# Optimization experiments

Hardware: AMD Instinct MI355X
Metric: run time of the kernel (lower is better)

The kernel has to match this reference:

```python
import jax, jax.numpy as jnp
import numpy as np

THRE = 4.0  # ReLUX threshold / multispike lens
EPS = 1e-5  # BatchNorm eps (torch default)

@jax.custom_vjp
def spike(x):
    # multispike forward: floor(clamp(x,0,4)+0.5)
    return jnp.floor(jnp.clip(x, 0.0, THRE) + 0.5)

def _spike_fwd(x):
    return spike(x), x

def _spike_bwd(x, g):
    # surrogate gradient: pass-through on 0 < x < lens
    return (g * ((x > 0) & (x < THRE)).astype(g.dtype),)

spike.defvjp(_spike_fwd, _spike_bwd)


def setup_inputs() -> dict:
    key = jax.random.key(0)
    k0, k1, k2 = jax.random.split(key, 3)
    B, N, C = 4, 1024, 512
    x = jax.random.normal(k0, (B, N, C), jnp.float32)
    Wqkv = jax.random.normal(k1, (3 * C, C), jnp.float32) * (C ** -0.5)  # Linear weight [out,in], no bias
    gamma = jnp.ones((3 * C,), jnp.float32)   # BN weight
    beta = jnp.zeros((3 * C,), jnp.float32)   # BN bias
    Wproj = jax.random.normal(k2, (C, C), jnp.float32) * (C ** -0.5)
    bproj = jnp.zeros((C,), jnp.float32)
    return {"x": x, "Wqkv": Wqkv, "gamma": gamma, "beta": beta, "Wproj": Wproj, "bproj": bproj}


def reference(x, Wqkv, gamma, beta, Wproj, bproj):
    B, N, C = x.shape
    H = 8
    hd = C // H
    scale = hd ** -0.5

    xs = spike(x)                                    # head_spike
    qkv = jnp.einsum('bnc,dc->bnd', xs, Wqkv)        # [B,N,3C]
    # BatchNorm1d over channel dim with batch stats across (B, N)
    mu = qkv.mean(axis=(0, 1))
    var = qkv.var(axis=(0, 1))
    qkv = (qkv - mu) * jax.lax.rsqrt(var + EPS) * gamma + beta

    qkv = qkv.reshape(B, N, 3, H, hd).transpose(2, 0, 3, 1, 4)  # [3,B,H,N,hd]
    q = spike(qkv[0])
    k = spike(qkv[1])
    v = spike(qkv[2])

    attn = jnp.einsum('bhnd,bhmd->bhnm', q, k)       # no softmax
    attn = spike(attn)
    out = jnp.einsum('bhnm,bhmd->bhnd', attn, v) * scale
    out = out.transpose(0, 2, 1, 3).reshape(B, N, C)
    out = spike(out)                                 # project_spike
    return jnp.einsum('bnc,dc->bnd', out, Wproj) + bproj
```

## Files before the change

### kernel.cpp

```cpp
#include <hip/hip_runtime.h>

typedef __attribute__((ext_vector_type(8))) short short8;
typedef __attribute__((ext_vector_type(4))) short short4v;
typedef __attribute__((ext_vector_type(8))) signed char s8x8;
typedef __attribute__((ext_vector_type(4))) unsigned char u8x4;
typedef __attribute__((ext_vector_type(4))) float f32x4;
typedef __attribute__((ext_vector_type(4))) int int4v;
typedef __attribute__((ext_vector_type(4))) unsigned int u32x4;

#define THRE 4.0f

#define GLOAD_LDS16(g, l) \
    __builtin_amdgcn_global_load_lds((const __attribute__((address_space(1))) void*)(g), \
                                     (__attribute__((address_space(3))) void*)(l), 16, 0, 0)

__device__ __forceinline__ float spikef(float x) {
    return floorf(fminf(fmaxf(x, 0.0f), THRE) + 0.5f);
}
__device__ __forceinline__ unsigned short f2bf(float f) {
    return (unsigned short)(__builtin_bit_cast(unsigned int, f) >> 16);
}
__device__ __forceinline__ unsigned short f2bf_rn(float f) {
    unsigned u = __builtin_bit_cast(unsigned int, f);
    unsigned r = ((u >> 16) & 1u) + 0x7FFFu;
    return (unsigned short)((u + r) >> 16);
}
__device__ __forceinline__ float bf2f(unsigned short s) {
    return __builtin_bit_cast(float, (unsigned int)s << 16);
}
__device__ __forceinline__ int4v mfma_i8(u32x4 a, u32x4 b, int4v c) {
    return __builtin_amdgcn_mfma_i32_16x16x64_i8(__builtin_bit_cast(int4v, a),
                                                 __builtin_bit_cast(int4v, b), c, 0, 0, 0);
}

__global__ void k_prep(const float* __restrict__ x,
                       const float* __restrict__ Wq, const float* __restrict__ Wp,
                       unsigned char* __restrict__ xs8, signed char* __restrict__ Wq8,
                       float* __restrict__ wscale, short* __restrict__ Wpd) {
    const int blk = blockIdx.x, tid = threadIdx.x;
    if (blk < 2048) {
        const int i = blk * 256 + tid;
        const float4 v = *(const float4*)&x[(size_t)i * 4];
        u8x4 o;
        o.x = (unsigned char)spikef(v.x);
        o.y = (unsigned char)spikef(v.y);
        o.z = (unsigned char)spikef(v.z);
        o.w = (unsigned char)spikef(v.w);
        *(u8x4*)&xs8[(size_t)i * 4] = o;
    } else if (blk < 2432) {
        const int row = (blk - 2048) * 4 + (tid >> 6);
        const int lane = tid & 63;
        const float* wr = Wq + (size_t)row * 512 + lane * 8;
        float w[8];
        float mx = 0.f;
        #pragma unroll
        for (int i = 0; i < 8; ++i) { w[i] = wr[i]; mx = fmaxf(mx, fabsf(w[i])); }
        #pragma unroll
        for (int o = 32; o > 0; o >>= 1) mx = fmaxf(mx, __shfl_xor(mx, o, 64));
        const float inv = mx > 0.f ? 127.0f / mx : 0.f;
        s8x8 q;
        #pragma unroll
        for (int i = 0; i < 8; ++i) q[i] = (signed char)rintf(w[i] * inv);
        *(s8x8*)&Wq8[(size_t)row * 512 + lane * 8] = q;
        if (lane == 0) wscale[row] = mx > 0.f ? mx / 127.0f : 0.f;
    } else {
        const int i = (blk - 2432) * 256 + tid;
        const float4 v = *(const float4*)&Wp[(size_t)i * 4];
        short4v o;
        o.x = (short)(__builtin_bit_cast(unsigned int, v.x) >> 16);
        o.y = (short)(__builtin_bit_cast(unsigned int, v.y) >> 16);
        o.z = (short)(__builtin_bit_cast(unsigned int, v.z) >> 16);
        o.w = (short)(__builtin_bit_cast(unsigned int, v.w) >> 16);
        *(short4v*)&Wpd[(size_t)i * 4] = o;
    }
}

__global__ __launch_bounds__(256) void k_gemm_qkv(const unsigned char* __restrict__ A,
                                                  const signed char* __restrict__ B,
                                                  const float* __restrict__ wscale,
                                                  short* __restrict__ C,
                                                  float* __restrict__ psum,
                                                  float* __restrict__ psq) {
    __shared__ __align__(16) unsigned char As[128 * 128];
    __shared__ __align__(16) unsigned char Bs[96 * 128];
    const int tid  = threadIdx.x;
    const int lane = tid & 63, wv = tid >> 6;
    const int wy = wv >> 1, wx = wv & 1;
    const int quad = lane >> 4, l16 = lane & 15;
    const int u = blockIdx.x;
    const int mtile = u & 31;
    const int m0 = mtile * 128, n0 = (u >> 5) * 96;
    const int N = 1536;

    int4v acc[4][3];
    #pragma unroll
    for (int i = 0; i < 4; ++i)
        #pragma unroll
        for (int j = 0; j < 3; ++j)
            #pragma unroll
            for (int r = 0; r < 4; ++r) acc[i][j][r] = 0;

    const unsigned char* gA[4]; unsigned char* lA[4];
    #pragma unroll
    for (int i = 0; i < 4; ++i) {
        int L = wv + 4 * i;
        int c = L * 64 + lane;
        int r = c >> 3, g = (c & 7) ^ (r & 7);
        gA[i] = A + (size_t)(m0 + r) * 512 + g * 16;
        lA[i] = &As[(size_t)c * 16];
    }
    const unsigned char* gB[3]; unsigned char* lB[3];
    #pragma unroll
    for (int i = 0; i < 3; ++i) {
        int L = wv + 4 * i;
        int c = L * 64 + lane;
        int r = c >> 3, g = (c & 7) ^ (r & 7);
        gB[i] = (const unsigned char*)B + (size_t)(n0 + r) * 512 + g * 16;
        lB[i] = &Bs[(size_t)c * 16];
    }

    for (int k0 = 0; k0 < 512; k0 += 128) {
        __syncthreads();
        #pragma unroll
        for (int i = 0; i < 4; ++i) GLOAD_LDS16(gA[i] + k0, lA[i]);
        #pragma unroll
        for (int i = 0; i < 3; ++i) GLOAD_LDS16(gB[i] + k0, lB[i]);
        __syncthreads();
        #pragma unroll
        for (int kk = 0; kk < 2; ++kk) {
            u32x4 aF[4], bF[3];
            #pragma unroll
            for (int mt = 0; mt < 4; ++mt) {
                const int r = wy * 64 + mt * 16 + l16;
                aF[mt] = *(const u32x4*)&As[(size_t)r * 128 + (((kk * 4 + quad) ^ (r & 7)) * 16)];
            }
            #pragma unroll
            for (int nt = 0; nt < 3; ++nt) {
                const int r = wx * 48 + nt * 16 + l16;
                bF[nt] = *(const u32x4*)&Bs[(size_t)r * 128 + (((kk * 4 + quad) ^ (r & 7)) * 16)];
            }
            #pragma unroll
            for (int mt = 0; mt < 4; ++mt)
                #pragma unroll
                for (int nt = 0; nt < 3; ++nt)
                    acc[mt][nt] = mfma_i8(aF[mt], bF[nt], acc[mt][nt]);
        }
    }

    float sc[3];
    #pragma unroll
    for (int nt = 0; nt < 3; ++nt) sc[nt] = wscale[n0 + wx * 48 + nt * 16 + l16];

    float vacc[4][3][4];
    #pragma unroll
    for (int mt = 0; mt < 4; ++mt)
        #pragma unroll
        for (int r = 0; r < 4; ++r) {
            int row = m0 + wy * 64 + mt * 16 + quad * 4 + r;
            short* Cr = C + (size_t)row * N + n0 + wx * 48 + l16;
            #pragma unroll
            for (int nt = 0; nt < 3; ++nt) {
                float v = (float)acc[mt][nt][r] * sc[nt];
                vacc[mt][nt][r] = v;
                Cr[nt * 16] = (short)f2bf_rn(v);
            }
        }

    __syncthreads();
    float* PS = (float*)As;
    float* PQ = (float*)Bs;
    #pragma unroll
    for (int nt = 0; nt < 3; ++nt) {
        float s = 0.f, q = 0.f;
        #pragma unroll
        for (int mt = 0; mt < 4; ++mt)
            #pragma unroll
            for (int r = 0; r < 4; ++r) {
                float v = vacc[mt][nt][r];
                s += v;
                q = fmaf(v, v, q);
            }
        PS[(wy * 4 + quad) * 96 + wx * 48 + nt * 16 + l16] = s;
        PQ[(wy * 4 + quad) * 96 + wx * 48 + nt * 16 + l16] = q;
    }
    __syncthreads();
    if (tid < 96) {
        float s = 0.f, q = 0.f;
        #pragma unroll
        for (int i = 0; i < 8; ++i) { s += PS[i * 96 + tid]; q += PQ[i * 96 + tid]; }
        psum[mtile * 1536 + n0 + tid] = s;
        psq [mtile * 1536 + n0 + tid] = q;
    }
}

__global__ __launch_bounds__(256) void k_gemm_proj(const short* __restrict__ A,
                                                   const short* __restrict__ B,
                                                   const float* __restrict__ bias,
                                                   float* __restrict__ C) {
    __shared__ __align__(16) short As[32 * 64];
    __shared__ __align__(16) short Bs[128 * 64];
    const int tid  = threadIdx.x;
    const int lane = tid & 63, wv = tid >> 6;
    const int wy = wv >> 1, wx = wv & 1;
    const int quad = lane >> 4, l16 = lane & 15;
    const int u = blockIdx.x;
    const int mtile = u & 127;
    const int m0 = mtile * 32, n0 = (u >> 7) * 128;
    const int K = 512, N = 512;

    f32x4 acc[4];
    #pragma unroll
    for (int j = 0; j < 4; ++j)
        #pragma unroll
        for (int r = 0; r < 4; ++r) acc[j][r] = 0.f;

    const short* gA0; short* lA0;
    {
        int c = tid;
        int r = c >> 3, g = (c & 7) ^ (r & 7);
        gA0 = A + (size_t)(m0 + r) * K + g * 8;
        lA0 = &As[(size_t)c * 8];
    }
    const short* gB[4]; short* lB[4];
    #pragma unroll
    for (int i = 0; i < 4; ++i) {
        int c = tid + 256 * i;
        int r = c >> 3, g = (c & 7) ^ (r & 7);
        gB[i] = B + (size_t)(n0 + r) * K + g * 8;
        lB[i] = &Bs[(size_t)c * 8];
    }

    for (int k0 = 0; k0 < K; k0 += 64) {
        __syncthreads();
        GLOAD_LDS16(gA0 + k0, lA0);
        #pragma unroll
        for (int i = 0; i < 4; ++i) GLOAD_LDS16(gB[i] + k0, lB[i]);
        __syncthreads();
        #pragma unroll
        for (int kk = 0; kk < 2; ++kk) {
            const int ra = wy * 16 + l16;
            short8 aF = *(const short8*)&As[(size_t)ra * 64 + (((kk * 4 + quad) ^ (ra & 7)) * 8)];
            #pragma unroll
            for (int nt = 0; nt < 4; ++nt) {
                const int rb = wx * 64 + nt * 16 + l16;
                short8 bF = *(const short8*)&Bs[(size_t)rb * 64 + (((kk * 4 + quad) ^ (rb & 7)) * 8)];
                acc[nt] = __builtin_amdgcn_mfma_f32_16x16x32_bf16(aF, bF, acc[nt], 0, 0, 0);
            }
        }
    }

    float bs[4];
    #pragma unroll
    for (int nt = 0; nt < 4; ++nt) bs[nt] = bias[n0 + wx * 64 + nt * 16 + l16];
    #pragma unroll
    for (int r = 0; r < 4; ++r) {
        int row = m0 + wy * 16 + quad * 4 + r;
        float* Cr = C + (size_t)row * N + n0 + wx * 64 + l16;
        #pragma unroll
        for (int nt = 0; nt < 4; ++nt) Cr[nt * 16] = acc[nt][r] + bs[nt];
    }
}

__global__ __launch_bounds__(256) void k_bn_spike(const short* __restrict__ qkvb,
                           const float* __restrict__ psum, const float* __restrict__ psq,
                           const float* __restrict__ gamma, const float* __restrict__ beta,
                           unsigned char* __restrict__ qp, unsigned char* __restrict__ kp,
                           unsigned char* __restrict__ vt) {
    __shared__ float sa[64], sb[64];
    __shared__ __align__(16) unsigned char tile[64 * 80];
    const int tid = threadIdx.x;
    const int slice = blockIdx.x;
    const int c0 = slice * 64;
    const int r0 = blockIdx.y * 256;
    const int b = r0 >> 10, nb = r0 & 1023;

    if (tid < 64) {
        const int c = c0 + tid;
        double s = 0.0, q = 0.0;
        for (int st = 0; st < 32; ++st) { s += (double)psum[st * 1536 + c]; q += (double)psq[st * 1536 + c]; }
        const double mu  = s / 4096.0;
        const double var = q / 4096.0 - mu * mu;
        const float a = (float)((double)gamma[c] / sqrt(var + 1e-5));
        sa[tid] = a;
        sb[tid] = fmaf(-(float)mu, a, beta[c]);
    }
    __syncthreads();

    if (slice < 16) {
        const int h = slice & 7;
        const int ch4 = (tid & 15) * 4, rr = tid >> 4;
        const float4 A4 = *(const float4*)&sa[ch4];
        const float4 B4 = *(const float4*)&sb[ch4];
        unsigned char* base = (slice < 8 ? qp : kp) + (((size_t)b * 8 + h) * 1024 + nb) * 64;
        for (int i = rr; i < 256; i += 16) {
            const short4v v4 = *(const short4v*)&qkvb[(size_t)(r0 + i) * 1536 + c0 + ch4];
            u8x4 o;
            o.x = (unsigned char)spikef(fmaf(bf2f((unsigned short)v4.x), A4.x, B4.x));
            o.y = (unsigned char)spikef(fmaf(bf2f((unsigned short)v4.y), A4.y, B4.y));
            o.z = (unsigned char)spikef(fmaf(bf2f((unsigned short)v4.z), A4.z, B4.z));
            o.w = (unsigned char)spikef(fmaf(bf2f((unsigned short)v4.w), A4.w, B4.w));
            *(u8x4*)&base[(size_t)i * 64 + ch4] = o;
        }
    } else {
        const int h = slice - 16;
        const int ch = tid & 63, rq = tid >> 6;
        const float A = sa[ch], Bsh = sb[ch];
        const int e = tid >> 2, j0 = (tid & 3) * 16;
        unsigned char* vbase = vt + (((size_t)b * 8 + h) * 64 + e) * 1024 + nb;
        for (int rb = 0; rb < 4; ++rb) {
            __syncthreads();
            for (int i = rq; i < 64; i += 4) {
                float v = bf2f((unsigned short)qkvb[(size_t)(r0 + rb * 64 + i) * 1536 + c0 + ch]);
                tile[ch * 80 + i] = (unsigned char)spikef(fmaf(v, A, Bsh));
            }
            __syncthreads();
            *(u32x4*)&vbase[rb * 64 + j0] = *(const u32x4*)&tile[e * 80 + j0];
        }
    }
}

__global__ __launch_bounds__(256) void k_attn(const unsigned char* __restrict__ qp,
                                              const unsigned char* __restrict__ kp,
                                              const unsigned char* __restrict__ vt,
                                              short* __restrict__ sout) {
    __shared__ __align__(16) unsigned char SM[54272];
    unsigned char* Qs = SM;
    unsigned char* Ks = SM + 4096;
    unsigned char* Vs = SM + 20480;
    unsigned int* Sb = (unsigned int*)(SM + 36864);
    const int tid  = threadIdx.x;
    const int lane = tid & 63, w = tid >> 6;
    const int quad = lane >> 4, l16 = lane & 15;
    const int u = blockIdx.x;
    const int bhid = u & 31;
    const int b = bhid >> 3, h = bhid & 7;
    const int n0 = (u >> 5) * 64;
    const size_t bh = (size_t)b * 8 + h;

    {
        const int r = tid >> 2, p = tid & 3;
        const int g = p ^ (r & 3) ^ ((r >> 2) & 3);
        GLOAD_LDS16(qp + (bh * 1024 + n0 + r) * 64 + g * 16, Qs + (size_t)tid * 16);
    }
    const unsigned char* gK[4]; unsigned char* lK[4];
    const unsigned char* gV[4]; unsigned char* lV[4];
    #pragma unroll
    for (int i = 0; i < 4; ++i) {
        int c = tid + 256 * i;
        int rk = c >> 2, pk2 = c & 3;
        int gk = pk2 ^ (rk & 3) ^ ((rk >> 2) & 3);
        gK[i] = kp + (bh * 1024 + rk) * 64 + gk * 16;
        lK[i] = Ks + (size_t)c * 16;
        int rv = c >> 4, pv = c & 15;
        int gv = pv ^ (rv & 15);
        gV[i] = vt + (bh * 64 + rv) * 1024 + gv * 16;
        lV[i] = Vs + (size_t)c * 16;
    }
    __syncthreads();
    u32x4 qf[4];
    {
        const int pq = quad ^ (l16 & 3) ^ ((l16 >> 2) & 3);
        #pragma unroll
        for (int mt = 0; mt < 4; ++mt)
            qf[mt] = *(const u32x4*)&Qs[(mt * 16 + l16) * 64 + pq * 16];
    }

    int4v of[4];
    #pragma unroll
    for (int mt = 0; mt < 4; ++mt)
        #pragma unroll
        for (int r = 0; r < 4; ++r) of[mt][r] = 0;

    const int pk = quad ^ (l16 & 3) ^ ((l16 >> 2) & 3);

    for (int j0 = 0; j0 < 1024; j0 += 256) {
        __syncthreads();
        #pragma unroll
        for (int i = 0; i < 4; ++i) {
            GLOAD_LDS16(gK[i] + (size_t)j0 * 64, lK[i]);
            GLOAD_LDS16(gV[i] + j0, lV[i]);
        }
        __syncthreads();

        #pragma unroll
        for (int jt = 0; jt < 4; ++jt) {
            u32x4 kf = *(const u32x4*)&Ks[(w * 64 + jt * 16 + l16) * 64 + pk * 16];
            #pragma unroll
            for (int mt = 0; mt < 4; ++mt) {
                int4v z;
                #pragma unroll
                for (int r = 0; r < 4; ++r) z[r] = 0;
                int4v s = mfma_i8(kf, qf[mt], z);
                unsigned int pkk = 0;
                #pragma unroll
                for (int r = 0; r < 4; ++r) {
                    int v = s[r]; v = v < 0 ? 0 : (v > 4 ? 4 : v);
                    pkk |= (unsigned int)v << (8 * r);
                }
                Sb[(mt * 16 + l16) * 68 + w * 16 + jt * 4 + quad] = pkk;
            }
        }
        __syncthreads();

        #pragma unroll
        for (int kk = 0; kk < 4; ++kk) {
            const int pv = (kk * 4 + quad) ^ l16;
            u32x4 bV = *(const u32x4*)&Vs[(w * 16 + l16) * 256 + pv * 16];
            #pragma unroll
            for (int mt = 0; mt < 4; ++mt) {
                u32x4 aS = *(const u32x4*)&Sb[(mt * 16 + l16) * 68 + kk * 16 + quad * 4];
                of[mt] = mfma_i8(aS, bV, of[mt]);
            }
        }
    }

    #pragma unroll
    for (int mt = 0; mt < 4; ++mt)
        #pragma unroll
        for (int r = 0; r < 4; ++r) {
            size_t orow = (size_t)b * 1024 + n0 + mt * 16 + quad * 4 + r;
            sout[orow * 512 + h * 64 + w * 16 + l16] =
                (short)f2bf(spikef((float)of[mt][r] * 0.125f));
        }
}

extern "C" void kernel_launch(void* const* d_in, const int* in_sizes, int n_in,
                              void* d_out, int out_size, void* d_ws, size_t ws_size,
                              hipStream_t stream) {
    const float* x     = (const float*)d_in[0];
    const float* Wqkv  = (const float*)d_in[1];
    const float* gamma = (const float*)d_in[2];
    const float* beta  = (const float*)d_in[3];
    const float* Wproj = (const float*)d_in[4];
    const float* bproj = (const float*)d_in[5];
    float* out = (float*)d_out;

    char* w = (char*)d_ws;
    unsigned char* xs8   = (unsigned char*)(w);
    signed char* Wq8     = (signed char*)(w + 8388608);
    float* wscale        = (float*)(w + 9437184);
    short* Wproj2        = (short*)(w + 11534336);
    short* qkvb          = (short*)(w + 12582912);
    unsigned char* qp    = (unsigned char*)(w + 37748736);
    unsigned char* kp    = (unsigned char*)(w + 41943040);
    unsigned char* vt    = (unsigned char*)(w + 46137344);
    float* psum          = (float*)(w + 50331648);
    float* psq           = psum + 32 * 1536;
    short* sout          = (short*)(w);

    k_prep<<<2688, 256, 0, stream>>>(x, Wqkv, Wproj, xs8, Wq8, wscale, Wproj2);
    k_gemm_qkv<<<512, 256, 0, stream>>>(xs8, Wq8, wscale, qkvb, psum, psq);
    k_bn_spike<<<dim3(24, 16), 256, 0, stream>>>(qkvb, psum, psq, gamma, beta, qp, kp, vt);
    k_attn<<<512, 256, 0, stream>>>(qp, kp, vt, sout);
    k_gemm_proj<<<512, 256, 0, stream>>>(sout, Wproj2, bproj, out);
}
```

Before: 110.3 us.

## Load K/V fragments directly from global into registers, double-buffer score tile

The attention kernel no longer stages Q, K and V through shared memory via global_load_lds. Each wave instead reads its MFMA fragments straight from global memory into registers, prefetching the next K chunk while the current one is processed. The V-transpose producer now writes V in a blocked layout that matches those register loads, and the score buffer is double-buffered with s_setprio hints around the MFMA sections. The Wproj bf16 conversion also switches from truncation to round-to-nearest. This removes LDS traffic and a pair of barriers per chunk, in exchange for more uncoalesced global loads and higher register pressure.

Result: no change. 108.9 us (-1.2%).

```diff
diff --git a/kernel.cpp b/kernel.cpp
--- a/kernel.cpp
+++ b/kernel.cpp
@@ -67,10 +67,10 @@
         const int i = (blk - 2432) * 256 + tid;
         const float4 v = *(const float4*)&Wp[(size_t)i * 4];
         short4v o;
-        o.x = (short)(__builtin_bit_cast(unsigned int, v.x) >> 16);
-        o.y = (short)(__builtin_bit_cast(unsigned int, v.y) >> 16);
-        o.z = (short)(__builtin_bit_cast(unsigned int, v.z) >> 16);
-        o.w = (short)(__builtin_bit_cast(unsigned int, v.w) >> 16);
+        o.x = (short)f2bf_rn(v.x);
+        o.y = (short)f2bf_rn(v.y);
+        o.z = (short)f2bf_rn(v.z);
+        o.w = (short)f2bf_rn(v.w);
         *(short4v*)&Wpd[(size_t)i * 4] = o;
     }
 }
@@ -306,7 +306,8 @@
         const int ch = tid & 63, rq = tid >> 6;
         const float A = sa[ch], Bsh = sb[ch];
         const int e = tid >> 2, j0 = (tid & 3) * 16;
-        unsigned char* vbase = vt + (((size_t)b * 8 + h) * 64 + e) * 1024 + nb;
+        unsigned char* vbase = vt + (size_t)b * 524288 + (size_t)h * 65536
+                             + (size_t)(nb >> 8) * 16384 + e * 64 + j0;
         for (int rb = 0; rb < 4; ++rb) {
             __syncthreads();
             for (int i = rq; i < 64; i += 4) {
@@ -314,7 +315,7 @@
                 tile[ch * 80 + i] = (unsigned char)spikef(fmaf(v, A, Bsh));
             }
             __syncthreads();
-            *(u32x4*)&vbase[rb * 64 + j0] = *(const u32x4*)&tile[e * 80 + j0];
+            *(u32x4*)&vbase[rb * 4096] = *(const u32x4*)&tile[e * 80 + j0];
         }
     }
 }
@@ -323,11 +324,7 @@
                                               const unsigned char* __restrict__ kp,
                                               const unsigned char* __restrict__ vt,
                                               short* __restrict__ sout) {
-    __shared__ __align__(16) unsigned char SM[54272];
-    unsigned char* Qs = SM;
-    unsigned char* Ks = SM + 4096;
-    unsigned char* Vs = SM + 20480;
-    unsigned int* Sb = (unsigned int*)(SM + 36864);
+    __shared__ __align__(16) unsigned int Sb[2][64 * 68];
     const int tid  = threadIdx.x;
     const int lane = tid & 63, w = tid >> 6;
     const int quad = lane >> 4, l16 = lane & 15;
@@ -337,33 +334,13 @@
     const int n0 = (u >> 5) * 64;
     const size_t bh = (size_t)b * 8 + h;
 
-    {
-        const int r = tid >> 2, p = tid & 3;
-        const int g = p ^ (r & 3) ^ ((r >> 2) & 3);
-        GLOAD_LDS16(qp + (bh * 1024 + n0 + r) * 64 + g * 16, Qs + (size_t)tid * 16);
-    }
-    const unsigned char* gK[4]; unsigned char* lK[4];
-    const unsigned char* gV[4]; unsigned char* lV[4];
-    #pragma unroll
-    for (int i = 0; i < 4; ++i) {
-        int c = tid + 256 * i;
-        int rk = c >> 2, pk2 = c & 3;
-        int gk = pk2 ^ (rk & 3) ^ ((rk >> 2) & 3);
-        gK[i] = kp + (bh * 1024 + rk) * 64 + gk * 16;
-        lK[i] = Ks + (size_t)c * 16;
-        int rv = c >> 4, pv = c & 15;
-        int gv = pv ^ (rv & 15);
-        gV[i] = vt + (bh * 64 + rv) * 1024 + gv * 16;
-        lV[i] = Vs + (size_t)c * 16;
-    }
-    __syncthreads();
+    const unsigned char* Kb = kp + bh * 65536;
+    const unsigned char* Vb = vt + bh * 65536;
+
     u32x4 qf[4];
-    {
-        const int pq = quad ^ (l16 & 3) ^ ((l16 >> 2) & 3);
-        #pragma unroll
-        for (int mt = 0; mt < 4; ++mt)
-            qf[mt] = *(const u32x4*)&Qs[(mt * 16 + l16) * 64 + pq * 16];
-    }
+    #pragma unroll
+    for (int mt = 0; mt < 4; ++mt)
+        qf[mt] = *(const u32x4*)&qp[(bh * 1024 + n0 + mt * 16 + l16) * 64 + quad * 16];
 
     int4v of[4];
     #pragma unroll
@@ -371,47 +348,55 @@
         #pragma unroll
         for (int r = 0; r < 4; ++r) of[mt][r] = 0;
 
-    const int pk = quad ^ (l16 & 3) ^ ((l16 >> 2) & 3);
-
-    for (int j0 = 0; j0 < 1024; j0 += 256) {
-        __syncthreads();
-        #pragma unroll
-        for (int i = 0; i < 4; ++i) {
-            GLOAD_LDS16(gK[i] + (size_t)j0 * 64, lK[i]);
-            GLOAD_LDS16(gV[i] + j0, lV[i]);
-        }
-        __syncthreads();
-
+    u32x4 kfc[4];
+    #pragma unroll
+    for (int jt = 0; jt < 4; ++jt)
+        kfc[jt] = *(const u32x4*)&Kb[(size_t)(w * 64 + jt * 16 + l16) * 64 + quad * 16];
+
+    #pragma unroll
+    for (int t = 0; t < 4; ++t) {
+        u32x4 bV[4];
+        #pragma unroll
+        for (int kk = 0; kk < 4; ++kk)
+            bV[kk] = *(const u32x4*)&Vb[(size_t)((t * 4 + kk) * 64 + w * 16 + l16) * 64 + quad * 16];
+
+        __builtin_amdgcn_s_setprio(1);
         #pragma unroll
         for (int jt = 0; jt < 4; ++jt) {
-            u32x4 kf = *(const u32x4*)&Ks[(w * 64 + jt * 16 + l16) * 64 + pk * 16];
             #pragma unroll
             for (int mt = 0; mt < 4; ++mt) {
                 int4v z;
                 #pragma unroll
                 for (int r = 0; r < 4; ++r) z[r] = 0;
-                int4v s = mfma_i8(kf, qf[mt], z);
+                int4v s = mfma_i8(kfc[jt], qf[mt], z);
                 unsigned int pkk = 0;
                 #pragma unroll
                 for (int r = 0; r < 4; ++r) {
                     int v = s[r]; v = v < 0 ? 0 : (v > 4 ? 4 : v);
                     pkk |= (unsigned int)v << (8 * r);
                 }
-                Sb[(mt * 16 + l16) * 68 + w * 16 + jt * 4 + quad] = pkk;
-            }
-        }
+                Sb[t & 1][(mt * 16 + l16) * 68 + w * 16 + jt * 4 + quad] = pkk;
+            }
+        }
+        __builtin_amdgcn_s_setprio(0);
         __syncthreads();
 
+        if (t < 3) {
+            #pragma unroll
+            for (int jt = 0; jt < 4; ++jt)
+                kfc[jt] = *(const u32x4*)&Kb[(size_t)((t + 1) * 256 + w * 64 + jt * 16 + l16) * 64 + quad * 16];
+        }
+
+        __builtin_amdgcn_s_setprio(1);
         #pragma unroll
         for (int kk = 0; kk < 4; ++kk) {
-            const int pv = (kk * 4 + quad) ^ l16;
-            u32x4 bV = *(const u32x4*)&Vs[(w * 16 + l16) * 256 + pv * 16];
             #pragma unroll
             for (int mt = 0; mt < 4; ++mt) {
-                u32x4 aS = *(const u32x4*)&Sb[(mt * 16 + l16) * 68 + kk * 16 + quad * 4];
-                of[mt] = mfma_i8(aS, bV, of[mt]);
-            }
-        }
+                u32x4 aS = *(const u32x4*)&Sb[t & 1][(mt * 16 + l16) * 68 + kk * 16 + quad * 4];
+                of[mt] = mfma_i8(aS, bV[kk], of[mt]);
+            }
+        }
+        __builtin_amdgcn_s_setprio(0);
     }
 
     #pragma unroll
```
